# Performance work log

Measured on AMD Instinct MI355X. Metric: run time of the kernel, lower is better.

Reference implementation:

```python
import jax, jax.numpy as jnp
import numpy as np

TAKE = 64
HID = 64


def setup_inputs() -> dict:
    key = jax.random.key(0)
    ks = jax.random.split(key, 12)
    B, N, C = 32, 1000, 1601
    s = 1.0 / np.sqrt(C)
    s2 = 1.0 / np.sqrt(HID)
    return {
        "class_logits": jax.random.normal(ks[0], (B, N, C), dtype=jnp.float32),
        "proposals": jax.random.uniform(ks[1], (B, N, 4), dtype=jnp.float32),
        # subject projection (Linear stored as [in, out] so y = x @ W + b)
        "Ws1": jax.random.uniform(ks[2], (C, HID), minval=-s, maxval=s),
        "bs1": jax.random.uniform(ks[3], (HID,), minval=-s, maxval=s),
        "Ws2": jax.random.uniform(ks[4], (HID, HID), minval=-s2, maxval=s2),
        "bs2": jax.random.uniform(ks[5], (HID,), minval=-s2, maxval=s2),
        # object projection
        "Wo1": jax.random.uniform(ks[6], (C, HID), minval=-s, maxval=s),
        "bo1": jax.random.uniform(ks[7], (HID,), minval=-s, maxval=s),
        "Wo2": jax.random.uniform(ks[8], (HID, HID), minval=-s2, maxval=s2),
        "bo2": jax.random.uniform(ks[9], (HID,), minval=-s2, maxval=s2),
    }


def _mlp(x, W1, b1, W2, b2):
    # Linear -> ReLU -> Linear
    return jnp.maximum(x @ W1 + b1, 0.0) @ W2 + b2


def reference(class_logits, proposals, Ws1, bs1, Ws2, bs2, Wo1, bo1, Wo2, bo2):
    B, N, _ = class_logits.shape
    subj = _mlp(class_logits, Ws1, bs1, Ws2, bs2)  # [B, N, 64]
    obj = _mlp(class_logits, Wo1, bo1, Wo2, bo2)   # [B, N, 64]
    # relatedness[b, i, j] = sigmoid(<subj_i, obj_j>)
    scores = jax.nn.sigmoid(jnp.einsum("bnd,bmd->bnm", subj, obj))  # [B, N, N]
    flat = scores.reshape(B, N * N)
    top_scores, top_idx = jax.lax.top_k(flat, TAKE)  # descending, same as sort[:take]
    # flat index k = subject*N + object (row-major), matching the torch meshgrid
    pairs = jnp.stack([top_idx // N, top_idx % N], axis=-1)  # [B, 64, 2] (subj, obj)
    return pairs, top_scores
```

## Files before the change

### kernel.cpp

```cpp
#include <hip/hip_runtime.h>
#include <cstdint>

#define NB 32
#define NN 1000
#define NC 1601
#define HID 64
#define ROWS (NB*NN)
#define CAPB 15360
#define SROWS 15
#define NBIN 4096
#define KCH 32
#define RB 64
#define TPB 128
#define XSTR 68
#define WSTR 132
#define SSTR 132

__device__ __forceinline__ uint32_t f2key(float f){
  uint32_t u = __float_as_uint(f);
  return (u & 0x80000000u) ? ~u : (u | 0x80000000u);
}
__device__ __forceinline__ float key2f(uint32_t k){
  uint32_t u = (k & 0x80000000u) ? (k & 0x7fffffffu) : ~k;
  return __uint_as_float(u);
}

__global__ __launch_bounds__(TPB, 1) void mlp_kernel(
    const float* __restrict__ x,
    const float* __restrict__ Ws1, const float* __restrict__ bs1,
    const float* __restrict__ Ws2, const float* __restrict__ bs2,
    const float* __restrict__ Wo1, const float* __restrict__ bo1,
    const float* __restrict__ Wo2, const float* __restrict__ bo2,
    float* __restrict__ subj, float* __restrict__ obj)
{
  __shared__ float smem[2*KCH*XSTR + 2*KCH*WSTR];
  __shared__ float xtail[RB];
  const int tid = threadIdx.x;
  const int tx  = tid & 15;
  const int ty  = tid >> 4;
  const int row0 = blockIdx.x * RB;

  float* xbuf = smem;
  float* wbuf = smem + 2*KCH*XSTR;

  float accS[8][4], accO[8][4];
  #pragma unroll
  for (int r=0;r<8;r++)
    #pragma unroll
    for (int c=0;c<4;c++){ accS[r][c]=0.f; accO[r][c]=0.f; }

  float  xstg[16];
  float4 wstg[8];
  #pragma unroll
  for (int it=0; it<16; it++){
    int u = tid + it*TPB;
    xstg[it] = x[(size_t)(row0 + (u>>5))*NC + (u&31)];
  }
  #pragma unroll
  for (int it=0; it<8; it++){
    int u = tid + it*TPB;
    int k = u>>5, c4 = u&31;
    const float* src = (c4 < 16) ? (Ws1 + (size_t)k*HID + c4*4)
                                 : (Wo1 + (size_t)k*HID + (c4-16)*4);
    wstg[it] = *(const float4*)src;
  }

  const int NCHUNK = 50;
  for (int c = 0; c < NCHUNK; c++){
    float* xT = xbuf + (c & 1)*(KCH*XSTR);
    float* wC = wbuf + (c & 1)*(KCH*WSTR);
    #pragma unroll
    for (int it=0; it<16; it++){
      int u = tid + it*TPB;
      xT[(u&31)*XSTR + (u>>5)] = xstg[it];
    }
    #pragma unroll
    for (int it=0; it<8; it++){
      int u = tid + it*TPB;
      *(float4*)&wC[(u>>5)*WSTR + (u&31)*4] = wstg[it];
    }
    __syncthreads();
    if (c+1 < NCHUNK){
      const int k0n = (c+1)*KCH;
      #pragma unroll
      for (int it=0; it<16; it++){
        int u = tid + it*TPB;
        xstg[it] = x[(size_t)(row0 + (u>>5))*NC + k0n + (u&31)];
      }
      #pragma unroll
      for (int it=0; it<8; it++){
        int u = tid + it*TPB;
        int k = u>>5, c4 = u&31;
        const float* src = (c4 < 16) ? (Ws1 + (size_t)(k0n+k)*HID + c4*4)
                                     : (Wo1 + (size_t)(k0n+k)*HID + (c4-16)*4);
        wstg[it] = *(const float4*)src;
      }
    }
    #pragma unroll 4
    for (int k=0; k<KCH; k++){
      float4 a0 = *(const float4*)&xT[k*XSTR + ty*8];
      float4 a1 = *(const float4*)&xT[k*XSTR + ty*8 + 4];
      float4 bS = *(const float4*)&wC[k*WSTR + tx*4];
      float4 bO = *(const float4*)&wC[k*WSTR + 64 + tx*4];
      float av[8] = {a0.x,a0.y,a0.z,a0.w,a1.x,a1.y,a1.z,a1.w};
      float bs_[4] = {bS.x,bS.y,bS.z,bS.w};
      float bo_[4] = {bO.x,bO.y,bO.z,bO.w};
      #pragma unroll
      for (int r=0;r<8;r++)
        #pragma unroll
        for (int c2=0;c2<4;c2++){
          accS[r][c2] = fmaf(av[r], bs_[c2], accS[r][c2]);
          accO[r][c2] = fmaf(av[r], bo_[c2], accO[r][c2]);
        }
    }
  }

  if (tid < RB) xtail[tid] = x[(size_t)(row0 + tid)*NC + 1600];
  __syncthreads();
  {
    float4 a0 = *(const float4*)&xtail[ty*8];
    float4 a1 = *(const float4*)&xtail[ty*8 + 4];
    float4 bS = *(const float4*)(Ws1 + (size_t)1600*HID + tx*4);
    float4 bO = *(const float4*)(Wo1 + (size_t)1600*HID + tx*4);
    float av[8] = {a0.x,a0.y,a0.z,a0.w,a1.x,a1.y,a1.z,a1.w};
    float bs_[4] = {bS.x,bS.y,bS.z,bS.w};
    float bo_[4] = {bO.x,bO.y,bO.z,bO.w};
    #pragma unroll
    for (int r=0;r<8;r++)
      #pragma unroll
      for (int c2=0;c2<4;c2++){
        accS[r][c2] = fmaf(av[r], bs_[c2], accS[r][c2]);
        accO[r][c2] = fmaf(av[r], bo_[c2], accO[r][c2]);
      }
  }

  float* hTS = smem;
  float* hTO = smem + 64*XSTR;
  __syncthreads();
  #pragma unroll
  for (int jj=0; jj<4; jj++){
    float bS = bs1[tx*4 + jj];
    float bO = bo1[tx*4 + jj];
    float4 h0, h1;
    h0.x = fmaxf(accS[0][jj]+bS, 0.f); h0.y = fmaxf(accS[1][jj]+bS, 0.f);
    h0.z = fmaxf(accS[2][jj]+bS, 0.f); h0.w = fmaxf(accS[3][jj]+bS, 0.f);
    h1.x = fmaxf(accS[4][jj]+bS, 0.f); h1.y = fmaxf(accS[5][jj]+bS, 0.f);
    h1.z = fmaxf(accS[6][jj]+bS, 0.f); h1.w = fmaxf(accS[7][jj]+bS, 0.f);
    *(float4*)&hTS[(tx*4+jj)*XSTR + ty*8]     = h0;
    *(float4*)&hTS[(tx*4+jj)*XSTR + ty*8 + 4] = h1;
    h0.x = fmaxf(accO[0][jj]+bO, 0.f); h0.y = fmaxf(accO[1][jj]+bO, 0.f);
    h0.z = fmaxf(accO[2][jj]+bO, 0.f); h0.w = fmaxf(accO[3][jj]+bO, 0.f);
    h1.x = fmaxf(accO[4][jj]+bO, 0.f); h1.y = fmaxf(accO[5][jj]+bO, 0.f);
    h1.z = fmaxf(accO[6][jj]+bO, 0.f); h1.w = fmaxf(accO[7][jj]+bO, 0.f);
    *(float4*)&hTO[(tx*4+jj)*XSTR + ty*8]     = h0;
    *(float4*)&hTO[(tx*4+jj)*XSTR + ty*8 + 4] = h1;
  }
  __syncthreads();

  float accYS[8][4], accYO[8][4];
  #pragma unroll
  for (int c2=0;c2<4;c2++){
    float bvS = bs2[tx*4 + c2];
    float bvO = bo2[tx*4 + c2];
    #pragma unroll
    for (int r=0;r<8;r++){ accYS[r][c2] = bvS; accYO[r][c2] = bvO; }
  }
  #pragma unroll 2
  for (int d=0; d<64; d++){
    float4 aS0 = *(const float4*)&hTS[d*XSTR + ty*8];
    float4 aS1 = *(const float4*)&hTS[d*XSTR + ty*8 + 4];
    float4 aO0 = *(const float4*)&hTO[d*XSTR + ty*8];
    float4 aO1 = *(const float4*)&hTO[d*XSTR + ty*8 + 4];
    float4 wS = *(const float4*)(Ws2 + (size_t)d*HID + tx*4);
    float4 wO = *(const float4*)(Wo2 + (size_t)d*HID + tx*4);
    float aS[8] = {aS0.x,aS0.y,aS0.z,aS0.w,aS1.x,aS1.y,aS1.z,aS1.w};
    float aO[8] = {aO0.x,aO0.y,aO0.z,aO0.w,aO1.x,aO1.y,aO1.z,aO1.w};
    float wSv[4] = {wS.x,wS.y,wS.z,wS.w};
    float wOv[4] = {wO.x,wO.y,wO.z,wO.w};
    #pragma unroll
    for (int r=0;r<8;r++)
      #pragma unroll
      for (int c2=0;c2<4;c2++){
        accYS[r][c2] = fmaf(aS[r], wSv[c2], accYS[r][c2]);
        accYO[r][c2] = fmaf(aO[r], wOv[c2], accYO[r][c2]);
      }
  }
  #pragma unroll
  for (int r=0;r<8;r++){
    *(float4*)&subj[(size_t)(row0 + ty*8 + r)*HID + tx*4] =
      make_float4(accYS[r][0], accYS[r][1], accYS[r][2], accYS[r][3]);
    *(float4*)&obj[(size_t)(row0 + ty*8 + r)*HID + tx*4] =
      make_float4(accYO[r][0], accYO[r][1], accYO[r][2], accYO[r][3]);
  }
}

__global__ __launch_bounds__(1024, 4) void sample_thresh(
    const float* __restrict__ subj, const float* __restrict__ obj,
    uint32_t* __restrict__ L)
{
  __shared__ float sRows[SROWS*HID];
  __shared__ uint32_t keys[SROWS*NN];
  __shared__ uint32_t hist[256];
  __shared__ uint32_t sb[2];
  const int b = blockIdx.x, tid = threadIdx.x;

  const float4* sp = (const float4*)(subj + (size_t)b*NN*HID);
  if (tid < SROWS*16) ((float4*)sRows)[tid] = sp[tid];
  __syncthreads();

  for (int j = tid; j < NN; j += 1024){
    const float4* op4 = (const float4*)(obj + ((size_t)b*NN + j)*HID);
    float4 o[16];
    #pragma unroll
    for (int q=0;q<16;q++) o[q] = op4[q];
    #pragma unroll 1
    for (int i=0;i<SROWS;i++){
      const float4* s4 = (const float4*)(sRows + i*HID);
      float acc = 0.f;
      #pragma unroll
      for (int q=0;q<16;q++){
        float4 s = s4[q];
        acc = fmaf(s.x, o[q].x, acc); acc = fmaf(s.y, o[q].y, acc);
        acc = fmaf(s.z, o[q].z, acc); acc = fmaf(s.w, o[q].w, acc);
      }
      keys[i*NN + j] = f2key(acc);
    }
  }
  __syncthreads();

  uint32_t prefix = 0; int remaining = 64;
  for (int round = 0; round < 2; round++){
    const int shift = 24 - round*8;
    if (tid < 256) hist[tid] = 0;
    __syncthreads();
    for (int idx = tid; idx < SROWS*NN; idx += 1024){
      uint32_t k = keys[idx];
      bool match = (round == 0) || ((k >> 24) == (prefix >> 24));
      if (match) atomicAdd(&hist[(k >> shift) & 255u], 1u);
    }
    __syncthreads();
    if (tid == 0){
      uint32_t cum = 0; int bin = 255;
      for (;; bin--){ cum += hist[bin]; if (cum >= (uint32_t)remaining || bin == 0) break; }
      sb[0] = (uint32_t)bin;
      sb[1] = (uint32_t)(remaining - (int)(cum - hist[bin]));
    }
    __syncthreads();
    prefix |= sb[0] << shift;
    remaining = (int)sb[1];
    __syncthreads();
  }
  if (tid == 0) L[b] = prefix;
}

__device__ __forceinline__ void score_tile_acc(
    const float* __restrict__ subj, const float* __restrict__ obj,
    int b, int ti, int tj, int tid,
    float* __restrict__ sT, float* __restrict__ oT, float (&acc)[8][8])
{
  const int tx = tid & 15, ty = tid >> 4;
  #pragma unroll
  for (int a=0;a<8;a++)
    #pragma unroll
    for (int c=0;c<8;c++) acc[a][c] = 0.f;

  #pragma unroll 1
  for (int half = 0; half < 2; half++){
    __syncthreads();
    {
      const float4* gp = (const float4*)subj;
      #pragma unroll
      for (int it=0; it<4; it++){
        int u = tid + it*256;
        int r = u >> 3, q = (u & 7) + half*8;
        int gr = b*NN + ti + r; gr = gr < ROWS ? gr : (ROWS-1);
        float4 v = gp[(size_t)gr*16 + q];
        int kk = (u & 7)*4;
        sT[(kk+0)*SSTR + r] = v.x;
        sT[(kk+1)*SSTR + r] = v.y;
        sT[(kk+2)*SSTR + r] = v.z;
        sT[(kk+3)*SSTR + r] = v.w;
      }
      const float4* gp2 = (const float4*)obj;
      #pragma unroll
      for (int it=0; it<4; it++){
        int u = tid + it*256;
        int r = u >> 3, q = (u & 7) + half*8;
        int gr = b*NN + tj + r; gr = gr < ROWS ? gr : (ROWS-1);
        float4 v = gp2[(size_t)gr*16 + q];
        int kk = (u & 7)*4;
        oT[(kk+0)*SSTR + r] = v.x;
        oT[(kk+1)*SSTR + r] = v.y;
        oT[(kk+2)*SSTR + r] = v.z;
        oT[(kk+3)*SSTR + r] = v.w;
      }
    }
    __syncthreads();
    #pragma unroll 2
    for (int k=0; k<32; k++){
      float4 s0 = *(const float4*)&sT[k*SSTR + ty*8];
      float4 s1 = *(const float4*)&sT[k*SSTR + ty*8 + 4];
      float4 o0 = *(const float4*)&oT[k*SSTR + tx*8];
      float4 o1 = *(const float4*)&oT[k*SSTR + tx*8 + 4];
      float s[8] = {s0.x,s0.y,s0.z,s0.w,s1.x,s1.y,s1.z,s1.w};
      float o[8] = {o0.x,o0.y,o0.z,o0.w,o1.x,o1.y,o1.z,o1.w};
      #pragma unroll
      for (int a=0;a<8;a++)
        #pragma unroll
        for (int c=0;c<8;c++)
          acc[a][c] = fmaf(s[a], o[c], acc[a][c]);
    }
  }
}

__global__ __launch_bounds__(256, 3) void score_pass1(
    const float* __restrict__ subj, const float* __restrict__ obj,
    const uint32_t* __restrict__ L, uint32_t* __restrict__ cnt,
    uint2* __restrict__ cand, uint32_t* __restrict__ ghist)
{
  __shared__ float sT[32*SSTR];
  __shared__ float oT[32*SSTR];
  __shared__ uint32_t hist[NBIN];
  __shared__ uint32_t lcnt, gbase;
  const int blk = blockIdx.x;
  const int b   = blk >> 6;
  const int t   = blk & 63;
  const int ti  = (t >> 3) << 7;
  const int tj  = (t & 7)  << 7;
  const int tid = threadIdx.x;
  const int tx = tid & 15, ty = tid >> 4;

  for (int i = tid; i < NBIN; i += 256) hist[i] = 0;
  if (tid == 0) lcnt = 0;

  float acc[8][8];
  score_tile_acc(subj, obj, b, ti, tj, tid, sT, oT, acc);

  const uint32_t Lb = L[b];
  int myCnt = 0;
  #pragma unroll
  for (int a=0;a<8;a++){
    int gi = ti + ty*8 + a;
    #pragma unroll
    for (int c=0;c<8;c++){
      int gj = tj + tx*8 + c;
      if (gi < NN && gj < NN){
        uint32_t key = f2key(acc[a][c]);
        if (key >= Lb){ myCnt++; atomicAdd(&hist[key >> 20], 1u); }
      }
    }
  }
  uint32_t lbase = atomicAdd(&lcnt, (uint32_t)myCnt);
  __syncthreads();
  if (tid == 0) gbase = atomicAdd(&cnt[b], lcnt);
  __syncthreads();
  uint32_t pos = gbase + lbase;
  #pragma unroll
  for (int a=0;a<8;a++){
    int gi = ti + ty*8 + a;
    #pragma unroll
    for (int c=0;c<8;c++){
      int gj = tj + tx*8 + c;
      if (gi < NN && gj < NN){
        uint32_t key = f2key(acc[a][c]);
        if (key >= Lb){
          if (pos < CAPB) cand[(size_t)b*CAPB + pos] = make_uint2(key, (uint32_t)(gi*NN + gj));
          pos++;
        }
      }
    }
  }
  __syncthreads();
  for (int i = tid; i < NBIN; i += 256){
    uint32_t v = hist[i];
    if (v) atomicAdd(&ghist[(size_t)b*NBIN + i], v);
  }
}

__global__ __launch_bounds__(256, 1) void pick_thresh(
    const uint32_t* __restrict__ ghist, const uint32_t* __restrict__ cnt,
    uint32_t* __restrict__ T, uint32_t* __restrict__ flag)
{
  __shared__ uint32_t S[256];
  const int b = blockIdx.x, tid = threadIdx.x;
  const uint32_t* h = ghist + (size_t)b*NBIN;
  uint32_t loc[16];
  uint32_t s = 0;
  #pragma unroll
  for (int i=0;i<16;i++){ loc[i] = h[tid*16 + i]; s += loc[i]; }
  S[tid] = s;
  __syncthreads();
  for (int off = 1; off < 256; off <<= 1){
    uint32_t v = (tid + off < 256) ? S[tid + off] : 0u;
    __syncthreads();
    S[tid] += v;
    __syncthreads();
  }
  uint32_t above = (tid < 255) ? S[tid + 1] : 0u;
  if (above < 64u && S[tid] >= 64u){
    uint32_t suf = above; int best = 0;
    for (int i=15;i>=0;i--){ suf += loc[i]; if (suf >= 64u){ best = i; break; } }
    T[b] = (uint32_t)(tid*16 + best) << 20;
  }
  if (tid == 0) flag[b] = (cnt[b] > (uint32_t)CAPB) ? 1u : 0u;
}

__global__ __launch_bounds__(256, 3) void score_repair(
    const float* __restrict__ subj, const float* __restrict__ obj,
    const uint32_t* __restrict__ T, const uint32_t* __restrict__ flag,
    uint32_t* __restrict__ cnt2, uint2* __restrict__ cand)
{
  const int blk = blockIdx.x;
  const int b   = blk >> 6;
  if (flag[b] == 0u) return;

  __shared__ float sT[32*SSTR];
  __shared__ float oT[32*SSTR];
  __shared__ uint32_t lcnt, gbase;
  const int t   = blk & 63;
  const int ti  = (t >> 3) << 7;
  const int tj  = (t & 7)  << 7;
  const int tid = threadIdx.x;
  const int tx = tid & 15, ty = tid >> 4;

  if (tid == 0) lcnt = 0;

  float acc[8][8];
  score_tile_acc(subj, obj, b, ti, tj, tid, sT, oT, acc);

  const uint32_t Tb = T[b];
  int myCnt = 0;
  #pragma unroll
  for (int a=0;a<8;a++){
    int gi = ti + ty*8 + a;
    #pragma unroll
    for (int c=0;c<8;c++){
      int gj = tj + tx*8 + c;
      if (gi < NN && gj < NN && f2key(acc[a][c]) >= Tb) myCnt++;
    }
  }
  uint32_t lbase = atomicAdd(&lcnt, (uint32_t)myCnt);
  __syncthreads();
  if (tid == 0) gbase = atomicAdd(&cnt2[b], lcnt);
  __syncthreads();
  uint32_t pos = gbase + lbase;
  #pragma unroll
  for (int a=0;a<8;a++){
    int gi = ti + ty*8 + a;
    #pragma unroll
    for (int c=0;c<8;c++){
      int gj = tj + tx*8 + c;
      if (gi < NN && gj < NN){
        uint32_t key = f2key(acc[a][c]);
        if (key >= Tb){
          if (pos < CAPB) cand[(size_t)b*CAPB + pos] = make_uint2(key, (uint32_t)(gi*NN + gj));
          pos++;
        }
      }
    }
  }
}

__global__ __launch_bounds__(1024, 4) void final_select(
    const uint32_t* __restrict__ cnt, const uint32_t* __restrict__ cnt2,
    const uint32_t* __restrict__ flag, const uint2* __restrict__ cand,
    float* __restrict__ out)
{
  __shared__ uint32_t keys[CAPB];
  __shared__ uint32_t hist[256];
  __shared__ uint32_t sb[2];
  __shared__ uint2 win[192];
  __shared__ uint32_t wn;
  const int b = blockIdx.x, tid = threadIdx.x;
  uint32_t n0 = flag[b] ? cnt2[b] : cnt[b];
  const int n = (n0 < (uint32_t)CAPB) ? (int)n0 : CAPB;

  for (int i = tid; i < n; i += 1024) keys[i] = cand[(size_t)b*CAPB + i].x;
  if (tid == 0) wn = 0;
  __syncthreads();

  uint32_t prefix = 0; int remaining = 64;
  for (int round = 0; round < 4; round++){
    const int shift = 24 - round*8;
    if (tid < 256) hist[tid] = 0;
    __syncthreads();
    for (int i = tid; i < n; i += 1024){
      uint32_t k = keys[i];
      bool match = (round == 0) || ((k >> (shift+8)) == (prefix >> (shift+8)));
      if (match) atomicAdd(&hist[(k >> shift) & 255u], 1u);
    }
    __syncthreads();
    if (tid == 0){
      uint32_t cum = 0; int bin = 255;
      for (;; bin--){ cum += hist[bin]; if (cum >= (uint32_t)remaining || bin == 0) break; }
      sb[0] = (uint32_t)bin;
      sb[1] = (uint32_t)(remaining - (int)(cum - hist[bin]));
    }
    __syncthreads();
    prefix |= sb[0] << shift;
    remaining = (int)sb[1];
    __syncthreads();
  }
  const uint32_t Tk = prefix;

  for (int i = tid; i < n; i += 1024){
    if (keys[i] >= Tk){
      uint32_t p = atomicAdd(&wn, 1u);
      if (p < 192u) win[p] = make_uint2(keys[i], cand[(size_t)b*CAPB + i].y);
    }
  }
  __syncthreads();
  const int m = (wn < 192u) ? (int)wn : 192;

  if (tid < m){
    const uint64_t me = ((uint64_t)win[tid].x << 32) | (uint64_t)(uint32_t)(~win[tid].y);
    int rank = 0;
    for (int s = 0; s < m; s++){
      uint64_t oth = ((uint64_t)win[s].x << 32) | (uint64_t)(uint32_t)(~win[s].y);
      rank += (oth > me) ? 1 : 0;
    }
    if (rank < 64){
      const uint32_t f = win[tid].y;
      const float d  = key2f(win[tid].x);
      const float sc = 1.0f / (1.0f + expf(-d));
      out[((size_t)b*64 + rank)*2 + 0] = (float)(f / NN);
      out[((size_t)b*64 + rank)*2 + 1] = (float)(f % NN);
      out[(size_t)NB*64*2 + (size_t)b*64 + rank] = sc;
    }
  }
}

extern "C" void kernel_launch(void* const* d_in, const int* in_sizes, int n_in,
                              void* d_out, int out_size, void* d_ws, size_t ws_size,
                              hipStream_t stream) {
  const float* x   = (const float*)d_in[0];
  const float* Ws1 = (const float*)d_in[2];
  const float* bs1 = (const float*)d_in[3];
  const float* Ws2 = (const float*)d_in[4];
  const float* bs2 = (const float*)d_in[5];
  const float* Wo1 = (const float*)d_in[6];
  const float* bo1 = (const float*)d_in[7];
  const float* Wo2 = (const float*)d_in[8];
  const float* bo2 = (const float*)d_in[9];
  float* out = (float*)d_out;

  char* ws = (char*)d_ws;
  float*    subj = (float*)ws;
  float*    objp = (float*)(ws + 8192000);
  uint32_t* L    = (uint32_t*)(ws + 16384000);
  uint32_t* cnt  = (uint32_t*)(ws + 16384128);
  uint32_t* cnt2 = (uint32_t*)(ws + 16384256);
  uint32_t* ghist= (uint32_t*)(ws + 16384384);
  uint32_t* T    = (uint32_t*)(ws + 16908672);
  uint32_t* flag = (uint32_t*)(ws + 16908800);
  uint2*    cand = (uint2*)   (ws + 16908928);

  hipMemsetAsync(cnt, 0, 128 + 128 + 524288, stream);

  mlp_kernel<<<ROWS/RB, TPB, 0, stream>>>(x, Ws1, bs1, Ws2, bs2,
                                          Wo1, bo1, Wo2, bo2, subj, objp);
  sample_thresh<<<NB, 1024, 0, stream>>>(subj, objp, L);
  score_pass1<<<NB*64, 256, 0, stream>>>(subj, objp, L, cnt, cand, ghist);
  pick_thresh<<<NB, 256, 0, stream>>>(ghist, cnt, T, flag);
  score_repair<<<NB*64, 256, 0, stream>>>(subj, objp, T, flag, cnt2, cand);
  final_select<<<NB, 1024, 0, stream>>>(cnt, cnt2, flag, cand, out);
}
```

Before: 732.2 us.

## Enlarge MLP row tile to 128 rows and fold workspace memset into sampling kernel

The first-layer MLP tile doubles to 128 rows with 256 threads and the K chunk halves to 16, so each weight chunk staged in shared memory is reused across twice as many rows. Because the hidden-activation buffer now fills all of shared memory, the second layer runs the subject and object heads one after the other in a loop. Separately, the hipMemsetAsync of the counters and histogram is dropped and `sample_thresh` zeroes them, saving one launch. The trade-off is half as many blocks (250) for the GPU's compute units, which may leave some units idle, plus a serialized second layer.

```diff
diff --git a/kernel.cpp b/kernel.cpp
--- a/kernel.cpp
+++ b/kernel.cpp
@@ -9,10 +9,10 @@
 #define CAPB 15360
 #define SROWS 15
 #define NBIN 4096
-#define KCH 32
-#define RB 64
-#define TPB 128
-#define XSTR 68
+#define KCH 16
+#define RB 128
+#define TPB 256
+#define XSTR 132
 #define WSTR 132
 #define SSTR 132
 
@@ -49,15 +49,15 @@
     #pragma unroll
     for (int c=0;c<4;c++){ accS[r][c]=0.f; accO[r][c]=0.f; }
 
-  float  xstg[16];
-  float4 wstg[8];
-  #pragma unroll
-  for (int it=0; it<16; it++){
+  float  xstg[8];
+  float4 wstg[2];
+  #pragma unroll
+  for (int it=0; it<8; it++){
     int u = tid + it*TPB;
-    xstg[it] = x[(size_t)(row0 + (u>>5))*NC + (u&31)];
-  }
-  #pragma unroll
-  for (int it=0; it<8; it++){
+    xstg[it] = x[(size_t)(row0 + (u>>4))*NC + (u&15)];
+  }
+  #pragma unroll
+  for (int it=0; it<2; it++){
     int u = tid + it*TPB;
     int k = u>>5, c4 = u&31;
     const float* src = (c4 < 16) ? (Ws1 + (size_t)k*HID + c4*4)
@@ -65,30 +65,30 @@
     wstg[it] = *(const float4*)src;
   }
 
-  const int NCHUNK = 50;
+  const int NCHUNK = 100;
   for (int c = 0; c < NCHUNK; c++){
     float* xT = xbuf + (c & 1)*(KCH*XSTR);
     float* wC = wbuf + (c & 1)*(KCH*WSTR);
     #pragma unroll
-    for (int it=0; it<16; it++){
-      int u = tid + it*TPB;
-      xT[(u&31)*XSTR + (u>>5)] = xstg[it];
-    }
-    #pragma unroll
     for (int it=0; it<8; it++){
       int u = tid + it*TPB;
+      xT[(u&15)*XSTR + (u>>4)] = xstg[it];
+    }
+    #pragma unroll
+    for (int it=0; it<2; it++){
+      int u = tid + it*TPB;
       *(float4*)&wC[(u>>5)*WSTR + (u&31)*4] = wstg[it];
     }
     __syncthreads();
     if (c+1 < NCHUNK){
       const int k0n = (c+1)*KCH;
       #pragma unroll
-      for (int it=0; it<16; it++){
+      for (int it=0; it<8; it++){
         int u = tid + it*TPB;
-        xstg[it] = x[(size_t)(row0 + (u>>5))*NC + k0n + (u&31)];
-      }
-      #pragma unroll
-      for (int it=0; it<8; it++){
+        xstg[it] = x[(size_t)(row0 + (u>>4))*NC + k0n + (u&15)];
+      }
+      #pragma unroll
+      for (int it=0; it<2; it++){
         int u = tid + it*TPB;
         int k = u>>5, c4 = u&31;
         const float* src = (c4 < 16) ? (Ws1 + (size_t)(k0n+k)*HID + c4*4)
@@ -134,75 +134,71 @@
       }
   }
 
-  float* hTS = smem;
-  float* hTO = smem + 64*XSTR;
-  __syncthreads();
-  #pragma unroll
-  for (int jj=0; jj<4; jj++){
-    float bS = bs1[tx*4 + jj];
-    float bO = bo1[tx*4 + jj];
-    float4 h0, h1;
-    h0.x = fmaxf(accS[0][jj]+bS, 0.f); h0.y = fmaxf(accS[1][jj]+bS, 0.f);
-    h0.z = fmaxf(accS[2][jj]+bS, 0.f); h0.w = fmaxf(accS[3][jj]+bS, 0.f);
-    h1.x = fmaxf(accS[4][jj]+bS, 0.f); h1.y = fmaxf(accS[5][jj]+bS, 0.f);
-    h1.z = fmaxf(accS[6][jj]+bS, 0.f); h1.w = fmaxf(accS[7][jj]+bS, 0.f);
-    *(float4*)&hTS[(tx*4+jj)*XSTR + ty*8]     = h0;
-    *(float4*)&hTS[(tx*4+jj)*XSTR + ty*8 + 4] = h1;
-    h0.x = fmaxf(accO[0][jj]+bO, 0.f); h0.y = fmaxf(accO[1][jj]+bO, 0.f);
-    h0.z = fmaxf(accO[2][jj]+bO, 0.f); h0.w = fmaxf(accO[3][jj]+bO, 0.f);
-    h1.x = fmaxf(accO[4][jj]+bO, 0.f); h1.y = fmaxf(accO[5][jj]+bO, 0.f);
-    h1.z = fmaxf(accO[6][jj]+bO, 0.f); h1.w = fmaxf(accO[7][jj]+bO, 0.f);
-    *(float4*)&hTO[(tx*4+jj)*XSTR + ty*8]     = h0;
-    *(float4*)&hTO[(tx*4+jj)*XSTR + ty*8 + 4] = h1;
-  }
-  __syncthreads();
-
-  float accYS[8][4], accYO[8][4];
-  #pragma unroll
-  for (int c2=0;c2<4;c2++){
-    float bvS = bs2[tx*4 + c2];
-    float bvO = bo2[tx*4 + c2];
-    #pragma unroll
-    for (int r=0;r<8;r++){ accYS[r][c2] = bvS; accYO[r][c2] = bvO; }
-  }
-  #pragma unroll 2
-  for (int d=0; d<64; d++){
-    float4 aS0 = *(const float4*)&hTS[d*XSTR + ty*8];
-    float4 aS1 = *(const float4*)&hTS[d*XSTR + ty*8 + 4];
-    float4 aO0 = *(const float4*)&hTO[d*XSTR + ty*8];
-    float4 aO1 = *(const float4*)&hTO[d*XSTR + ty*8 + 4];
-    float4 wS = *(const float4*)(Ws2 + (size_t)d*HID + tx*4);
-    float4 wO = *(const float4*)(Wo2 + (size_t)d*HID + tx*4);
-    float aS[8] = {aS0.x,aS0.y,aS0.z,aS0.w,aS1.x,aS1.y,aS1.z,aS1.w};
-    float aO[8] = {aO0.x,aO0.y,aO0.z,aO0.w,aO1.x,aO1.y,aO1.z,aO1.w};
-    float wSv[4] = {wS.x,wS.y,wS.z,wS.w};
-    float wOv[4] = {wO.x,wO.y,wO.z,wO.w};
+  float* hT = smem;
+  #pragma unroll 1
+  for (int head = 0; head < 2; head++){
+    const float* b1 = head ? bo1 : bs1;
+    const float* b2 = head ? bo2 : bs2;
+    const float* W2 = head ? Wo2 : Ws2;
+    float* yout     = head ? obj : subj;
+    __syncthreads();
+    #pragma unroll
+    for (int jj=0; jj<4; jj++){
+      float bias = b1[tx*4 + jj];
+      float4 h0, h1;
+      h0.x = fmaxf((head?accO[0][jj]:accS[0][jj]) + bias, 0.f);
+      h0.y = fmaxf((head?accO[1][jj]:accS[1][jj]) + bias, 0.f);
+      h0.z = fmaxf((head?accO[2][jj]:accS[2][jj]) + bias, 0.f);
+      h0.w = fmaxf((head?accO[3][jj]:accS[3][jj]) + bias, 0.f);
+      h1.x = fmaxf((head?accO[4][jj]:accS[4][jj]) + bias, 0.f);
+      h1.y = fmaxf((head?accO[5][jj]:accS[5][jj]) + bias, 0.f);
+      h1.z = fmaxf((head?accO[6][jj]:accS[6][jj]) + bias, 0.f);
+      h1.w = fmaxf((head?accO[7][jj]:accS[7][jj]) + bias, 0.f);
+      *(float4*)&hT[(tx*4+jj)*XSTR + ty*8]     = h0;
+      *(float4*)&hT[(tx*4+jj)*XSTR + ty*8 + 4] = h1;
+    }
+    __syncthreads();
+    float accY[8][4];
+    #pragma unroll
+    for (int c2=0;c2<4;c2++){
+      float bv = b2[tx*4 + c2];
+      #pragma unroll
+      for (int r=0;r<8;r++) accY[r][c2] = bv;
+    }
+    #pragma unroll 4
+    for (int d=0; d<64; d++){
+      float4 a0 = *(const float4*)&hT[d*XSTR + ty*8];
+      float4 a1 = *(const float4*)&hT[d*XSTR + ty*8 + 4];
+      float4 w  = *(const float4*)(W2 + (size_t)d*HID + tx*4);
+      float av[8] = {a0.x,a0.y,a0.z,a0.w,a1.x,a1.y,a1.z,a1.w};
+      float wv[4] = {w.x,w.y,w.z,w.w};
+      #pragma unroll
+      for (int r=0;r<8;r++)
+        #pragma unroll
+        for (int c2=0;c2<4;c2++)
+          accY[r][c2] = fmaf(av[r], wv[c2], accY[r][c2]);
+    }
     #pragma unroll
     for (int r=0;r<8;r++)
-      #pragma unroll
-      for (int c2=0;c2<4;c2++){
-        accYS[r][c2] = fmaf(aS[r], wSv[c2], accYS[r][c2]);
-        accYO[r][c2] = fmaf(aO[r], wOv[c2], accYO[r][c2]);
-      }
-  }
-  #pragma unroll
-  for (int r=0;r<8;r++){
-    *(float4*)&subj[(size_t)(row0 + ty*8 + r)*HID + tx*4] =
-      make_float4(accYS[r][0], accYS[r][1], accYS[r][2], accYS[r][3]);
-    *(float4*)&obj[(size_t)(row0 + ty*8 + r)*HID + tx*4] =
-      make_float4(accYO[r][0], accYO[r][1], accYO[r][2], accYO[r][3]);
+      *(float4*)&yout[(size_t)(row0 + ty*8 + r)*HID + tx*4] =
+        make_float4(accY[r][0], accY[r][1], accY[r][2], accY[r][3]);
   }
 }
 
 __global__ __launch_bounds__(1024, 4) void sample_thresh(
     const float* __restrict__ subj, const float* __restrict__ obj,
-    uint32_t* __restrict__ L)
+    uint32_t* __restrict__ L, uint32_t* __restrict__ cnt,
+    uint32_t* __restrict__ cnt2, uint32_t* __restrict__ ghist)
 {
   __shared__ float sRows[SROWS*HID];
   __shared__ uint32_t keys[SROWS*NN];
   __shared__ uint32_t hist[256];
   __shared__ uint32_t sb[2];
   const int b = blockIdx.x, tid = threadIdx.x;
+
+  uint32_t* gh = ghist + (size_t)b*NBIN;
+  for (int i = tid; i < NBIN; i += 1024) gh[i] = 0u;
+  if (tid == 0){ cnt[b] = 0u; cnt2[b] = 0u; }
 
   const float4* sp = (const float4*)(subj + (size_t)b*NN*HID);
   if (tid < SROWS*16) ((float4*)sRows)[tid] = sp[tid];
@@ -555,11 +551,9 @@
   uint32_t* flag = (uint32_t*)(ws + 16908800);
   uint2*    cand = (uint2*)   (ws + 16908928);
 
-  hipMemsetAsync(cnt, 0, 128 + 128 + 524288, stream);
-
   mlp_kernel<<<ROWS/RB, TPB, 0, stream>>>(x, Ws1, bs1, Ws2, bs2,
                                           Wo1, bo1, Wo2, bo2, subj, objp);
-  sample_thresh<<<NB, 1024, 0, stream>>>(subj, objp, L);
+  sample_thresh<<<NB, 1024, 0, stream>>>(subj, objp, L, cnt, cnt2, ghist);
   score_pass1<<<NB*64, 256, 0, stream>>>(subj, objp, L, cnt, cand, ghist);
   pick_thresh<<<NB, 256, 0, stream>>>(ghist, cnt, T, flag);
   score_repair<<<NB*64, 256, 0, stream>>>(subj, objp, T, flag, cnt2, cand);
```

After: 788.0 us. 1.08x slower.
